# Performance work log

Measured on AMD Instinct MI355X. Metric: run time of the kernel, lower is better.

## Reference

```python
import jax, jax.numpy as jnp
import numpy as np

N_NODES = 100000
N_EDGES = 3_200_000
F_IN, HID, N_CLS = 512, 16, 16


def setup_inputs() -> dict:
    key = jax.random.key(0)
    k1, k2, k3, k4 = jax.random.split(key, 4)
    x = jax.random.normal(k1, (N_NODES, F_IN), dtype=jnp.float32)
    edge_index = jax.random.randint(k2, (2, N_EDGES), 0, N_NODES, dtype=jnp.int64)
    W1 = jax.random.normal(k3, (F_IN, HID), dtype=jnp.float32) * 0.05
    b1 = jnp.zeros((HID,), dtype=jnp.float32)
    W2 = jax.random.normal(k4, (HID, N_CLS), dtype=jnp.float32) * 0.05
    b2 = jnp.zeros((N_CLS,), dtype=jnp.float32)
    return {"x": x, "edge_index": edge_index, "W1": W1, "b1": b1, "W2": W2, "b2": b2}


def _gcn_conv(x, W, b, row, col, norm, n_nodes):
    # GCNConv: linear first, then symmetric-normalized scatter-add aggregation
    h = x @ W                              # [N, out]
    msg = h[row] * norm[:, None]           # gather + scale, [E+N, out]
    out = jax.ops.segment_sum(msg, col, num_segments=n_nodes)
    return out + b


def reference(x, edge_index, W1, b1, W2, b2):
    n = x.shape[0]
    # add self-loops (GCNConv default)
    loop = jnp.arange(n, dtype=edge_index.dtype)
    row = jnp.concatenate([edge_index[0], loop])
    col = jnp.concatenate([edge_index[1], loop])
    # symmetric normalization D^-1/2 A D^-1/2 with edge_weight = 1
    deg = jax.ops.segment_sum(jnp.ones_like(col, dtype=x.dtype), col, num_segments=n)
    dinv = jnp.where(deg > 0, deg ** -0.5, 0.0)
    norm = dinv[row] * dinv[col]

    h = jax.nn.relu(_gcn_conv(x, W1, b1, row, col, norm, n))
    # dropout is identity in eval mode
    out = _gcn_conv(h, W2, b2, row, col, norm, n)
    return jax.nn.log_softmax(out, axis=-1)
```

## Files before the change

### kernel.cpp

```cpp
#include <hip/hip_runtime.h>
#include <hip/hip_fp16.h>

#define F_IN 512
#define BKT_BITS 7
#define NPB (1 << BKT_BITS)
#define NBMAX 1024
#define BWIN 5120
#define EPT 16
#define EPW (256 * EPT)

__global__ void k_init(int* __restrict__ cursor, int nb) {
    int i = blockIdx.x * blockDim.x + threadIdx.x;
    if (i < nb) cursor[i] = i * BWIN;
}

__global__ __launch_bounds__(256) void k_part(
    const int* __restrict__ row, const int* __restrict__ col,
    int* __restrict__ cursor, unsigned int* __restrict__ pairs, int E, int nb)
{
    __shared__ int hist[NBMAX];
    __shared__ int base[NBMAX];
    int tid = threadIdx.x;
    int e0 = blockIdx.x * EPW;
    for (int i = tid; i < nb; i += 256) hist[i] = 0;
    __syncthreads();
    int4 c4[EPT / 4];
    int rank[EPT];
    #pragma unroll
    for (int k = 0; k < EPT / 4; ++k) {
        int e = e0 + (tid + k * 256) * 4;
        if (e + 3 < E) {
            c4[k] = ((const int4*)col)[e >> 2];
        } else {
            c4[k].x = (e     < E) ? col[e]     : -1;
            c4[k].y = (e + 1 < E) ? col[e + 1] : -1;
            c4[k].z = (e + 2 < E) ? col[e + 2] : -1;
            c4[k].w = (e + 3 < E) ? col[e + 3] : -1;
        }
        const int* cc = (const int*)&c4[k];
        #pragma unroll
        for (int i = 0; i < 4; ++i)
            rank[4 * k + i] = (cc[i] >= 0) ? atomicAdd(&hist[cc[i] >> BKT_BITS], 1) : 0;
    }
    __syncthreads();
    for (int i = tid; i < nb; i += 256)
        base[i] = hist[i] ? atomicAdd(&cursor[i], hist[i]) : 0;
    __syncthreads();
    #pragma unroll
    for (int k = 0; k < EPT / 4; ++k) {
        int e = e0 + (tid + k * 256) * 4;
        int4 r4;
        if (e + 3 < E) {
            r4 = ((const int4*)row)[e >> 2];
        } else {
            r4.x = (e     < E) ? row[e]     : 0;
            r4.y = (e + 1 < E) ? row[e + 1] : 0;
            r4.z = (e + 2 < E) ? row[e + 2] : 0;
            r4.w = (e + 3 < E) ? row[e + 3] : 0;
        }
        const int* cc = (const int*)&c4[k];
        const int* rr = (const int*)&r4;
        #pragma unroll
        for (int i = 0; i < 4; ++i) {
            if (e + i >= E || cc[i] < 0) continue;
            int b = cc[i] >> BKT_BITS;
            int slot = b * BWIN + min(rank[4 * k + i] +
                       (int)0, BWIN - 1);
            slot = b * BWIN;
            int s2 = slot + (base[b] - slot) + rank[4 * k + i];
            if (s2 < (b + 1) * BWIN)
                pairs[s2] = ((unsigned int)rr[i] << BKT_BITS)
                          | (unsigned int)(cc[i] & (NPB - 1));
        }
    }
}

__global__ __launch_bounds__(256) void k_csr(
    unsigned int* __restrict__ pairs, const int* __restrict__ cursor,
    int2* __restrict__ pd, float* __restrict__ dinv, int n, int nb)
{
    __shared__ int hist[NPB];
    __shared__ int sc[NPB];
    __shared__ int curs[NPB];
    int b = blockIdx.x, tid = threadIdx.x;
    int n0 = b << BKT_BITS;
    int w0 = b * BWIN;
    int ec = min(cursor[b] - w0, BWIN);
    if (tid < NPB) hist[tid] = 0;
    __syncthreads();
    uint4 pv4[BWIN / 1024];
    #pragma unroll
    for (int k = 0; k < BWIN / 1024; ++k) {
        pv4[k] = ((const uint4*)(pairs + w0))[tid + k * 256];
        int e = (tid + k * 256) * 4;
        const unsigned int* pp = (const unsigned int*)&pv4[k];
        #pragma unroll
        for (int i = 0; i < 4; ++i)
            if (e + i < ec) atomicAdd(&hist[pp[i] & (NPB - 1)], 1);
    }
    __syncthreads();
    if (tid < NPB) sc[tid] = hist[tid];
    __syncthreads();
    for (int off = 1; off < NPB; off <<= 1) {
        int t = (tid < NPB && tid >= off) ? sc[tid - off] : 0;
        __syncthreads();
        if (tid < NPB) sc[tid] += t;
        __syncthreads();
    }
    if (tid < NPB) {
        int st = sc[tid] - hist[tid];
        curs[tid] = st;
        int node = n0 + tid;
        if (node < n) {
            pd[node] = make_int2(w0 + st, hist[tid]);
            dinv[node] = rsqrtf((float)(hist[tid] + 1));
        }
    }
    __syncthreads();
    #pragma unroll
    for (int k = 0; k < BWIN / 1024; ++k) {
        int e = (tid + k * 256) * 4;
        const unsigned int* pp = (const unsigned int*)&pv4[k];
        #pragma unroll
        for (int i = 0; i < 4; ++i) {
            if (e + i < ec) {
                unsigned int p = pp[i];
                int pos = atomicAdd(&curs[p & (NPB - 1)], 1);
                ((int*)pairs)[w0 + pos] = (int)(p >> BKT_BITS);
            }
        }
    }
}

__global__ __launch_bounds__(256) void k_gemm1(
    const float* __restrict__ x, const float* __restrict__ W1,
    const float* __restrict__ dinv, __half2* __restrict__ hs, int n)
{
    __shared__ float red[4][64 * 17];
    const int lane = threadIdx.x & 63;
    const int wib  = threadIdx.x >> 6;
    const int wave = blockIdx.x * 4 + wib;
    const int nw   = gridDim.x * 4;
    float* rb = red[wib];

    float w[128];
    #pragma unroll
    for (int i = 0; i < 32; ++i) {
        float4 t = ((const float4*)W1)[lane * 32 + i];
        w[4*i+0] = t.x; w[4*i+1] = t.y; w[4*i+2] = t.z; w[4*i+3] = t.w;
    }
    const int q  = lane >> 4;
    const int jj = lane & 15;

    int node = wave;
    float4 a = {}, b = {};
    float di = 0.f;
    if (node < n) {
        const float4* xr = (const float4*)(x + (size_t)node * F_IN);
        a = xr[lane * 2];
        b = xr[lane * 2 + 1];
        di = dinv[node];
    }
    while (node < n) {
        int nxt = node + nw;
        float4 an = {}, bn = {};
        float dn = 0.f;
        if (nxt < n) {
            const float4* xr = (const float4*)(x + (size_t)nxt * F_IN);
            an = xr[lane * 2];
            bn = xr[lane * 2 + 1];
            dn = dinv[nxt];
        }
        float xs[8] = {a.x, a.y, a.z, a.w, b.x, b.y, b.z, b.w};
        float p[16];
        #pragma unroll
        for (int j = 0; j < 16; ++j) p[j] = 0.f;
        #pragma unroll
        for (int i = 0; i < 8; ++i)
            #pragma unroll
            for (int j = 0; j < 16; ++j)
                p[j] = fmaf(xs[i], w[i * 16 + j], p[j]);

        #pragma unroll
        for (int j = 0; j < 16; ++j) rb[lane * 17 + j] = p[j];
        __asm__ volatile("s_waitcnt lgkmcnt(0)" ::: "memory");
        float s = 0.f;
        #pragma unroll
        for (int i = 0; i < 16; ++i) s += rb[(q * 16 + i) * 17 + jj];
        s += __shfl_down(s, 32);
        s += __shfl_down(s, 16);

        float sv = s * di;
        float sn = __shfl_down(sv, 1);
        if (lane < 16 && (lane & 1) == 0) {
            __half2 hv = __halves2half2(__float2half(sv), __float2half(sn));
            hs[node * 8 + (lane >> 1)] = hv;
        }
        node = nxt; a = an; b = bn; di = dn;
    }
}

__global__ __launch_bounds__(256) void k_agg1(
    const __half2* __restrict__ hs, const int2* __restrict__ pd,
    const int* __restrict__ csr, const float* __restrict__ dinv,
    const float* __restrict__ b1, const float* __restrict__ W2,
    __half2* __restrict__ hs2, int n)
{
    int t = blockIdx.x * blockDim.x + threadIdx.x;
    int node = t >> 3, j2 = t & 7;
    if (node >= n) return;
    int2 p = pd[node];
    int e = p.x, s1 = p.x + p.y;
    float2 sum = __half22float2(hs[node * 8 + j2]);
    for (; e + 8 <= s1; e += 8) {
        int a0 = csr[e],   a1 = csr[e+1], a2 = csr[e+2], a3 = csr[e+3];
        int a4 = csr[e+4], a5 = csr[e+5], a6 = csr[e+6], a7 = csr[e+7];
        float2 v0 = __half22float2(hs[a0 * 8 + j2]);
        float2 v1 = __half22float2(hs[a1 * 8 + j2]);
        float2 v2 = __half22float2(hs[a2 * 8 + j2]);
        float2 v3 = __half22float2(hs[a3 * 8 + j2]);
        float2 v4 = __half22float2(hs[a4 * 8 + j2]);
        float2 v5 = __half22float2(hs[a5 * 8 + j2]);
        float2 v6 = __half22float2(hs[a6 * 8 + j2]);
        float2 v7 = __half22float2(hs[a7 * 8 + j2]);
        sum.x += ((v0.x+v1.x)+(v2.x+v3.x)) + ((v4.x+v5.x)+(v6.x+v7.x));
        sum.y += ((v0.y+v1.y)+(v2.y+v3.y)) + ((v4.y+v5.y)+(v6.y+v7.y));
    }
    for (; e < s1; ++e) {
        float2 v = __half22float2(hs[csr[e] * 8 + j2]);
        sum.x += v.x; sum.y += v.y;
    }
    float di = dinv[node];
    float2 b1v = ((const float2*)b1)[j2];
    float va = fmaxf(fmaf(sum.x, di, b1v.x), 0.f);
    float vb = fmaxf(fmaf(sum.y, di, b1v.y), 0.f);
    float ha = 0.f, hb = 0.f;
    #pragma unroll
    for (int k2 = 0; k2 < 8; ++k2) {
        float oa = __shfl(va, k2, 8);
        float ob = __shfl(vb, k2, 8);
        ha = fmaf(oa, W2[(2*k2)   * 16 + 2*j2],     ha);
        hb = fmaf(oa, W2[(2*k2)   * 16 + 2*j2 + 1], hb);
        ha = fmaf(ob, W2[(2*k2+1) * 16 + 2*j2],     ha);
        hb = fmaf(ob, W2[(2*k2+1) * 16 + 2*j2 + 1], hb);
    }
    hs2[node * 8 + j2] = __halves2half2(__float2half(ha * di), __float2half(hb * di));
}

__global__ __launch_bounds__(256) void k_agg2(
    const __half2* __restrict__ hs2, const int2* __restrict__ pd,
    const int* __restrict__ csr, const float* __restrict__ dinv,
    const float* __restrict__ b2, float2* __restrict__ out, int n)
{
    int t = blockIdx.x * blockDim.x + threadIdx.x;
    int node = t >> 3, j2 = t & 7;
    if (node >= n) return;
    int2 p = pd[node];
    int e = p.x, s1 = p.x + p.y;
    float2 sum = __half22float2(hs2[node * 8 + j2]);
    for (; e + 8 <= s1; e += 8) {
        int a0 = csr[e],   a1 = csr[e+1], a2 = csr[e+2], a3 = csr[e+3];
        int a4 = csr[e+4], a5 = csr[e+5], a6 = csr[e+6], a7 = csr[e+7];
        float2 v0 = __half22float2(hs2[a0 * 8 + j2]);
        float2 v1 = __half22float2(hs2[a1 * 8 + j2]);
        float2 v2 = __half22float2(hs2[a2 * 8 + j2]);
        float2 v3 = __half22float2(hs2[a3 * 8 + j2]);
        float2 v4 = __half22float2(hs2[a4 * 8 + j2]);
        float2 v5 = __half22float2(hs2[a5 * 8 + j2]);
        float2 v6 = __half22float2(hs2[a6 * 8 + j2]);
        float2 v7 = __half22float2(hs2[a7 * 8 + j2]);
        sum.x += ((v0.x+v1.x)+(v2.x+v3.x)) + ((v4.x+v5.x)+(v6.x+v7.x));
        sum.y += ((v0.y+v1.y)+(v2.y+v3.y)) + ((v4.y+v5.y)+(v6.y+v7.y));
    }
    for (; e < s1; ++e) {
        float2 v = __half22float2(hs2[csr[e] * 8 + j2]);
        sum.x += v.x; sum.y += v.y;
    }
    float di = dinv[node];
    float2 b2v = ((const float2*)b2)[j2];
    float vx = fmaf(sum.x, di, b2v.x);
    float vy = fmaf(sum.y, di, b2v.y);
    float m = fmaxf(vx, vy);
    #pragma unroll
    for (int off = 4; off >= 1; off >>= 1) m = fmaxf(m, __shfl_xor(m, off));
    float s = expf(vx - m) + expf(vy - m);
    #pragma unroll
    for (int off = 4; off >= 1; off >>= 1) s += __shfl_xor(s, off);
    float ls = logf(s);
    out[node * 8 + j2] = make_float2(vx - m - ls, vy - m - ls);
}

extern "C" void kernel_launch(void* const* d_in, const int* in_sizes, int n_in,
                              void* d_out, int out_size, void* d_ws, size_t ws_size,
                              hipStream_t stream)
{
    const float* x  = (const float*)d_in[0];
    const int*   ei = (const int*)d_in[1];
    const float* W1 = (const float*)d_in[2];
    const float* b1 = (const float*)d_in[3];
    const float* W2 = (const float*)d_in[4];
    const float* b2 = (const float*)d_in[5];
    float* out = (float*)d_out;

    const int n = in_sizes[0] / F_IN;
    const int E = in_sizes[1] / 2;
    const int nb = (n + NPB - 1) >> BKT_BITS;

    char* ws = (char*)d_ws;
    size_t o = 0;
    #define ALIGN512(s) (((s) + 511) & ~(size_t)511)
    float* dinv = (float*)(ws + o);           o += ALIGN512((size_t)n * 4);
    int2*  pd   = (int2*)(ws + o);            o += ALIGN512((size_t)n * 8);
    int*   curs = (int*)(ws + o);             o += ALIGN512((size_t)NBMAX * 4);
    unsigned int* pairs = (unsigned int*)(ws + o);
    o += ALIGN512((size_t)nb * BWIN * 4);
    __half2* hs  = (__half2*)(ws + o);        o += ALIGN512((size_t)n * 16 * 2);
    __half2* hs2 = (__half2*)(ws + o);        o += ALIGN512((size_t)n * 16 * 2);
    #undef ALIGN512

    k_init<<<(nb + 255) / 256, 256, 0, stream>>>(curs, nb);
    k_part<<<(E + EPW - 1) / EPW, 256, 0, stream>>>(ei, ei + E, curs, pairs, E, nb);
    k_csr <<<nb, 256, 0, stream>>>(pairs, curs, pd, dinv, n, nb);

    k_gemm1<<<2048, 256, 0, stream>>>(x, W1, dinv, hs, n);
    k_agg1 <<<(n * 8 + 255) / 256, 256, 0, stream>>>(hs, pd, (const int*)pairs,
                                                     dinv, b1, W2, hs2, n);
    k_agg2 <<<(n * 8 + 255) / 256, 256, 0, stream>>>(hs2, pd, (const int*)pairs,
                                                     dinv, b2, (float2*)out, n);
}
```

Baseline: 465.5 us.

## Stage partitioned edges in LDS for coalesced bucket writes in partition and CSR

```diff
diff --git a/kernel.cpp b/kernel.cpp
--- a/kernel.cpp
+++ b/kernel.cpp
@@ -6,7 +6,7 @@
 #define NPB (1 << BKT_BITS)
 #define NBMAX 1024
 #define BWIN 5120
-#define EPT 16
+#define EPT 32
 #define EPW (256 * EPT)
 
 __global__ void k_init(int* __restrict__ cursor, int nb) {
@@ -18,12 +18,18 @@
     const int* __restrict__ row, const int* __restrict__ col,
     int* __restrict__ cursor, unsigned int* __restrict__ pairs, int E, int nb)
 {
+    __shared__ unsigned int staged[EPW];
+    __shared__ unsigned short bkt[EPW];
     __shared__ int hist[NBMAX];
+    __shared__ int sc[NBMAX];
     __shared__ int base[NBMAX];
+    __shared__ int wsum[4];
     int tid = threadIdx.x;
+    int lane = tid & 63;
     int e0 = blockIdx.x * EPW;
     for (int i = tid; i < nb; i += 256) hist[i] = 0;
     __syncthreads();
+
     int4 c4[EPT / 4];
     int rank[EPT];
     #pragma unroll
@@ -43,9 +49,39 @@
             rank[4 * k + i] = (cc[i] >= 0) ? atomicAdd(&hist[cc[i] >> BKT_BITS], 1) : 0;
     }
     __syncthreads();
-    for (int i = tid; i < nb; i += 256)
-        base[i] = hist[i] ? atomicAdd(&cursor[i], hist[i]) : 0;
-    __syncthreads();
+
+    int i0 = tid * 4;
+    int a0 = 0, a1 = 0, a2 = 0, a3 = 0;
+    {
+        int h0 = (i0     < nb) ? hist[i0]     : 0;
+        int h1 = (i0 + 1 < nb) ? hist[i0 + 1] : 0;
+        int h2 = (i0 + 2 < nb) ? hist[i0 + 2] : 0;
+        int h3 = (i0 + 3 < nb) ? hist[i0 + 3] : 0;
+        base[i0]     = h0 ? atomicAdd(&cursor[i0],     h0) : 0;
+        if (i0 + 1 < NBMAX) base[i0 + 1] = h1 ? atomicAdd(&cursor[i0 + 1], h1) : 0;
+        if (i0 + 2 < NBMAX) base[i0 + 2] = h2 ? atomicAdd(&cursor[i0 + 2], h2) : 0;
+        if (i0 + 3 < NBMAX) base[i0 + 3] = h3 ? atomicAdd(&cursor[i0 + 3], h3) : 0;
+        a0 = h0; a1 = h1; a2 = h2; a3 = h3;
+    }
+    int s = a0 + a1 + a2 + a3;
+    int ws = s;
+    #pragma unroll
+    for (int off = 1; off < 64; off <<= 1) {
+        int t = __shfl_up(ws, off);
+        if (lane >= off) ws += t;
+    }
+    if (lane == 63) wsum[tid >> 6] = ws;
+    __syncthreads();
+    int woff = 0;
+    #pragma unroll
+    for (int k = 0; k < 4; ++k) woff += (k < (tid >> 6)) ? wsum[k] : 0;
+    int excl = woff + ws - s;
+    sc[i0]     = excl + a0;
+    sc[i0 + 1] = excl + a0 + a1;
+    sc[i0 + 2] = excl + a0 + a1 + a2;
+    sc[i0 + 3] = excl + s;
+    __syncthreads();
+
     #pragma unroll
     for (int k = 0; k < EPT / 4; ++k) {
         int e = e0 + (tid + k * 256) * 4;
@@ -64,14 +100,20 @@
         for (int i = 0; i < 4; ++i) {
             if (e + i >= E || cc[i] < 0) continue;
             int b = cc[i] >> BKT_BITS;
-            int slot = b * BWIN + min(rank[4 * k + i] +
-                       (int)0, BWIN - 1);
-            slot = b * BWIN;
-            int s2 = slot + (base[b] - slot) + rank[4 * k + i];
-            if (s2 < (b + 1) * BWIN)
-                pairs[s2] = ((unsigned int)rr[i] << BKT_BITS)
-                          | (unsigned int)(cc[i] & (NPB - 1));
-        }
+            int pos = (sc[b] - hist[b]) + rank[4 * k + i];
+            staged[pos] = ((unsigned int)rr[i] << BKT_BITS)
+                        | (unsigned int)(cc[i] & (NPB - 1));
+            bkt[pos] = (unsigned short)b;
+        }
+    }
+    __syncthreads();
+
+    int vcnt = sc[nb - 1];
+    for (int i = tid; i < vcnt; i += 256) {
+        int b = bkt[i];
+        int gpos = base[b] + (i - (sc[b] - hist[b]));
+        if (gpos < (b + 1) * BWIN)
+            pairs[gpos] = staged[i];
     }
 }
 
@@ -79,6 +121,7 @@
     unsigned int* __restrict__ pairs, const int* __restrict__ cursor,
     int2* __restrict__ pd, float* __restrict__ dinv, int n, int nb)
 {
+    __shared__ int sorted[BWIN];
     __shared__ int hist[NPB];
     __shared__ int sc[NPB];
     __shared__ int curs[NPB];
@@ -88,12 +131,10 @@
     int ec = min(cursor[b] - w0, BWIN);
     if (tid < NPB) hist[tid] = 0;
     __syncthreads();
-    uint4 pv4[BWIN / 1024];
-    #pragma unroll
-    for (int k = 0; k < BWIN / 1024; ++k) {
-        pv4[k] = ((const uint4*)(pairs + w0))[tid + k * 256];
-        int e = (tid + k * 256) * 4;
-        const unsigned int* pp = (const unsigned int*)&pv4[k];
+    for (int e4 = tid; e4 < BWIN / 4; e4 += 256) {
+        uint4 p4 = ((const uint4*)(pairs + w0))[e4];
+        int e = e4 * 4;
+        const unsigned int* pp = (const unsigned int*)&p4;
         #pragma unroll
         for (int i = 0; i < 4; ++i)
             if (e + i < ec) atomicAdd(&hist[pp[i] & (NPB - 1)], 1);
@@ -117,19 +158,22 @@
         }
     }
     __syncthreads();
-    #pragma unroll
-    for (int k = 0; k < BWIN / 1024; ++k) {
-        int e = (tid + k * 256) * 4;
-        const unsigned int* pp = (const unsigned int*)&pv4[k];
+    for (int e4 = tid; e4 < BWIN / 4; e4 += 256) {
+        uint4 p4 = ((const uint4*)(pairs + w0))[e4];
+        int e = e4 * 4;
+        const unsigned int* pp = (const unsigned int*)&p4;
         #pragma unroll
         for (int i = 0; i < 4; ++i) {
             if (e + i < ec) {
                 unsigned int p = pp[i];
                 int pos = atomicAdd(&curs[p & (NPB - 1)], 1);
-                ((int*)pairs)[w0 + pos] = (int)(p >> BKT_BITS);
+                sorted[pos] = (int)(p >> BKT_BITS);
             }
         }
     }
+    __syncthreads();
+    for (int i = tid; i < ec; i += 256)
+        ((int*)pairs)[w0 + i] = sorted[i];
 }
 
 __global__ __launch_bounds__(256) void k_gemm1(
```

Measured after the change: 434.7 us. 1.07x faster.
